# Optimization experiments

Measured on AMD Instinct MI355X. Metric: run time of the kernel, lower is better.

Reference implementation:

```python
import jax, jax.numpy as jnp
from jax import lax
import numpy as np

B, C_IN, H, W = 8, 1024, 64, 64
DI, C_OUT = 512, 1024
BN_EPS = 1e-5


def setup_inputs() -> dict:
    key = jax.random.key(0)
    ks = jax.random.split(key, 5)
    std = 0.01  # torch init.normal_(std=0.01)
    return {
        "x": jax.random.normal(ks[0], (B, C_IN, H, W), jnp.float32),
        "theta_w": jax.random.normal(ks[1], (DI, C_IN), jnp.float32) * std,
        "theta_b": jnp.zeros((DI,), jnp.float32),
        "phi_w": jax.random.normal(ks[2], (DI, C_IN), jnp.float32) * std,
        "phi_b": jnp.zeros((DI,), jnp.float32),
        "g_w": jax.random.normal(ks[3], (DI, C_IN), jnp.float32) * std,
        "g_b": jnp.zeros((DI,), jnp.float32),
        "out_w": jax.random.normal(ks[4], (C_OUT, DI), jnp.float32) * std,
        "out_b": jnp.zeros((C_OUT,), jnp.float32),
        "bn_w": jnp.ones((C_OUT,), jnp.float32),
        "bn_b": jnp.zeros((C_OUT,), jnp.float32),
    }


def _conv1x1(x, w, b):
    # x: [b,c,h,w], w: [o,c] -> [b,o,h,w]
    return jnp.einsum('bchw,oc->bohw', x, w) + b[None, :, None, None]


def reference(x, theta_w, theta_b, phi_w, phi_b, g_w, g_b, out_w, out_b, bn_w, bn_b):
    b, c, h, w = x.shape
    di = theta_w.shape[0]

    theta = _conv1x1(x, theta_w, theta_b).reshape(b, di, h * w)  # [b,di,N]

    # MaxPool2d(kernel=2, stride=2)
    pool = lax.reduce_window(x, -jnp.inf, lax.max,
                             (1, 1, 2, 2), (1, 1, 2, 2), 'VALID')
    phi = _conv1x1(pool, phi_w, phi_b).reshape(b, di, -1)   # [b,di,M]
    g = _conv1x1(pool, g_w, g_b).reshape(b, di, -1)          # [b,di,M]

    # scaled dot-product attention: scores [b,N,M]
    scores = jnp.einsum('bdn,bdm->bnm', theta, phi) * (di ** -0.5)
    p = jax.nn.softmax(scores, axis=-1)

    # t_x = g @ p^T  -> [b,di,N]
    t = jnp.einsum('bdm,bnm->bdn', g, p).reshape(b, di, h, w)

    y = _conv1x1(t, out_w, out_b)  # [b,C_out,h,w]

    # BatchNorm2d (training mode: batch statistics, biased variance)
    mean = jnp.mean(y, axis=(0, 2, 3), keepdims=True)
    var = jnp.var(y, axis=(0, 2, 3), keepdims=True)
    y = (y - mean) * lax.rsqrt(var + BN_EPS)
    y = y * bn_w[None, :, None, None] + bn_b[None, :, None, None]

    return y + x
```

## Files before the change

kernel.cpp:

```cpp
#include <hip/hip_runtime.h>
#include <cstdint>

typedef unsigned short u16;
typedef __attribute__((ext_vector_type(4))) unsigned short u16x4;
typedef __attribute__((ext_vector_type(8))) short short8;
typedef __attribute__((ext_vector_type(4))) float f32x4;

#define DI 512
#define CIN 1024
#define NPIX 4096
#define MPIX 1024

__device__ __forceinline__ float bf2f(u16 u) {
  union { unsigned int i; float f; } v; v.i = ((unsigned int)u) << 16; return v.f;
}
__device__ __forceinline__ u16 f2bf(float f) {
  union { float f; unsigned int i; } v; v.f = f;
  unsigned int r = v.i + 0x7fffu + ((v.i >> 16) & 1u);
  return (u16)(r >> 16);
}
__device__ __forceinline__ void unpack8(uint4 v, float* f) {
  union { unsigned int i; float f; } u;
  u.i = v.x << 16;          f[0] = u.f;
  u.i = v.x & 0xffff0000u;  f[1] = u.f;
  u.i = v.y << 16;          f[2] = u.f;
  u.i = v.y & 0xffff0000u;  f[3] = u.f;
  u.i = v.z << 16;          f[4] = u.f;
  u.i = v.z & 0xffff0000u;  f[5] = u.f;
  u.i = v.w << 16;          f[6] = u.f;
  u.i = v.w & 0xffff0000u;  f[7] = u.f;
}

__device__ __forceinline__ void gload16(const u16* g, u16* l) {
  __builtin_amdgcn_global_load_lds(
      (const __attribute__((address_space(1))) void*)g,
      (__attribute__((address_space(3))) void*)l, 16, 0, 0);
}

__global__ __launch_bounds__(256) void cvt4_kernel(
    const float* __restrict__ s0, const float* __restrict__ s1,
    const float* __restrict__ s2, const float* __restrict__ s3,
    u16* __restrict__ d0, u16* __restrict__ d1,
    u16* __restrict__ d2, u16* __restrict__ d3) {
  int i = blockIdx.x * 256 + threadIdx.x;
  int sel = i >> 17;
  int j = i & 131071;
  const float* src = sel == 0 ? s0 : sel == 1 ? s1 : sel == 2 ? s2 : s3;
  u16* dst = sel == 0 ? d0 : sel == 1 ? d1 : sel == 2 ? d2 : d3;
  float4 v = *(const float4*)(src + (long)j * 4);
  u16x4 w;
  w[0] = f2bf(v.x); w[1] = f2bf(v.y); w[2] = f2bf(v.z); w[3] = f2bf(v.w);
  *(u16x4*)(dst + (long)j * 4) = w;
}

__global__ __launch_bounds__(256) void transpose_kernel(const float* __restrict__ x,
                                                        u16* __restrict__ xT) {
  __shared__ u16 tile[64][72];
  const int b = blockIdx.z;
  const int n0 = blockIdx.x * 64, c0 = blockIdx.y * 64;
  const float* xb = x + (long)b * CIN * NPIX;
  u16* xTb = xT + (long)b * NPIX * CIN;
  const int t = threadIdx.x;
  const int tc = t >> 4, tn = (t & 15) * 4;
  #pragma unroll
  for (int i = 0; i < 4; i++) {
    int c = tc + i * 16;
    float4 v = *(const float4*)(xb + (long)(c0 + c) * NPIX + n0 + tn);
    tile[c][tn + 0] = f2bf(v.x);
    tile[c][tn + 1] = f2bf(v.y);
    tile[c][tn + 2] = f2bf(v.z);
    tile[c][tn + 3] = f2bf(v.w);
  }
  __syncthreads();
  const int tn2 = t >> 4, tc2 = (t & 15) * 4;
  #pragma unroll
  for (int i = 0; i < 4; i++) {
    int n = tn2 + i * 16;
    u16x4 w;
    w[0] = tile[tc2 + 0][n];
    w[1] = tile[tc2 + 1][n];
    w[2] = tile[tc2 + 2][n];
    w[3] = tile[tc2 + 3][n];
    *(u16x4*)(xTb + (long)(n0 + n) * CIN + c0 + tc2) = w;
  }
}

__global__ __launch_bounds__(256) void pool_kernel(const u16* __restrict__ xT,
                                                   u16* __restrict__ poolT) {
  const int idx = blockIdx.x * 256 + threadIdx.x;
  const int cc = (idx & 127) * 8;
  const int m = (idx >> 7) & 1023;
  const int b = idx >> 17;
  const int i = m >> 5, j = m & 31;
  const int n1 = (i * 2) * 64 + j * 2;
  const u16* base = xT + (long)b * NPIX * CIN + cc;
  uint4 v0 = *(const uint4*)(base + (long)(n1) * CIN);
  uint4 v1 = *(const uint4*)(base + (long)(n1 + 1) * CIN);
  uint4 v2 = *(const uint4*)(base + (long)(n1 + 64) * CIN);
  uint4 v3 = *(const uint4*)(base + (long)(n1 + 65) * CIN);
  float f0[8], f1[8], f2[8], f3[8];
  unpack8(v0, f0); unpack8(v1, f1); unpack8(v2, f2); unpack8(v3, f3);
  u16 r[8] __attribute__((aligned(16)));
  #pragma unroll
  for (int k = 0; k < 8; k++) {
    float mx = fmaxf(fmaxf(f0[k], f1[k]), fmaxf(f2[k], f3[k]));
    r[k] = f2bf(mx);
  }
  *(uint4*)(poolT + ((long)b * MPIX + m) * CIN + cc) = *(uint4*)r;
}

template<int OM, bool HAS_BIAS, bool HAS_CS, bool HAS_SHIFT, bool HAS_EXP>
__global__ __launch_bounds__(256)
void gemm_tn(const u16* __restrict__ A, const u16* __restrict__ B,
             void* __restrict__ Cv,
             const float* __restrict__ bias, long sBias,
             const float* __restrict__ cs, long sCS,
             const float* __restrict__ shift, long sShift,
             float* __restrict__ psum_out,
             float scale, int M, int N, int K, long sA, long sB, long sC)
{
  A += blockIdx.z * sA;
  B += blockIdx.z * sB;
  if (HAS_BIAS) bias += blockIdx.z * sBias;
  if (HAS_CS) cs += blockIdx.z * sCS;
  if (HAS_SHIFT) shift += blockIdx.z * sShift;
  const int bm = blockIdx.y * 128;
  const int bn = blockIdx.x * 128;
  __shared__ __align__(16) u16 As[128 * 64];
  __shared__ __align__(16) u16 Bs[128 * 64];
  __shared__ float psum[2][128];
  const int tid = threadIdx.x;
  const int lane = tid & 63;
  const int wave = tid >> 6;
  const int wm = (wave >> 1) * 64;
  const int wn = (wave & 1) * 64;
  const int lr = lane & 15;
  const int q  = lane >> 4;
  const int sxor = lane & 7;
  f32x4 acc[4][4] = {};

  const int swz = ((lane & 7) ^ (lane >> 3)) * 8;
  const long grow = 32 * wave + (lane >> 3);
  const u16* Ag = A + ((long)bm + grow) * K + swz;
  const u16* Bg = B + ((long)bn + grow) * K + swz;

  for (int kt = 0; kt < K; kt += 64) {
    __syncthreads();
    #pragma unroll
    for (int i = 0; i < 4; i++) {
      gload16(Ag + (long)(8 * i) * K + kt, &As[(wave * 4 + i) * 512]);
      gload16(Bg + (long)(8 * i) * K + kt, &Bs[(wave * 4 + i) * 512]);
    }
    __syncthreads();
    #pragma unroll
    for (int kk = 0; kk < 2; kk++) {
      short8 av[4], bv[4];
      #pragma unroll
      for (int mi = 0; mi < 4; mi++)
        av[mi] = *(const short8*)&As[(wm + mi * 16 + lr) * 64 +
                                     (((kk << 2) + q) ^ sxor) * 8];
      #pragma unroll
      for (int ni = 0; ni < 4; ni++)
        bv[ni] = *(const short8*)&Bs[(wn + ni * 16 + lr) * 64 +
                                     (((kk << 2) + q) ^ sxor) * 8];
      #pragma unroll
      for (int mi = 0; mi < 4; mi++) {
        #pragma unroll
        for (int ni = 0; ni < 4; ni++)
          acc[mi][ni] = __builtin_amdgcn_mfma_f32_16x16x32_bf16(
              av[mi], bv[ni], acc[mi][ni], 0, 0, 0);
      }
    }
  }

  const int dr = (lane >> 4) * 4;
  float rowsum[4][4];
  if (HAS_EXP) {
    #pragma unroll
    for (int mi = 0; mi < 4; mi++)
      #pragma unroll
      for (int r = 0; r < 4; r++) rowsum[mi][r] = 0.f;
  }
  #pragma unroll
  for (int mi = 0; mi < 4; mi++) {
    const int rowb = bm + wm + mi * 16 + dr;
    float bvs[4] = {0.f, 0.f, 0.f, 0.f};
    float shv[4] = {0.f, 0.f, 0.f, 0.f};
    if (HAS_BIAS) {
      #pragma unroll
      for (int r = 0; r < 4; r++) bvs[r] = bias[rowb + r];
    }
    if (HAS_SHIFT) {
      #pragma unroll
      for (int r = 0; r < 4; r++) shv[r] = shift[rowb + r];
    }
    #pragma unroll
    for (int ni = 0; ni < 4; ni++) {
      const int col = bn + wn + ni * 16 + lr;
      const float csv = HAS_CS ? cs[col] : 1.0f;
      float v[4];
      #pragma unroll
      for (int r = 0; r < 4; r++) {
        float t = acc[mi][ni][r] * scale;
        if (HAS_CS) t *= csv;
        if (HAS_SHIFT) t -= shv[r];
        if (HAS_BIAS) t += bvs[r];
        if (HAS_EXP) { t = expf(t); rowsum[mi][r] += t; }
        v[r] = t;
      }
      if (OM == 1) {
        u16* C = (u16*)Cv + blockIdx.z * sC;
        u16x4 w;
        #pragma unroll
        for (int r = 0; r < 4; r++) w[r] = f2bf(v[r]);
        *(u16x4*)(C + (long)col * M + rowb) = w;
      } else if (OM == 0) {
        u16* C = (u16*)Cv + blockIdx.z * sC;
        #pragma unroll
        for (int r = 0; r < 4; r++)
          C[(long)(rowb + r) * N + col] = f2bf(v[r]);
      } else {
        float* C = (float*)Cv + blockIdx.z * sC;
        #pragma unroll
        for (int r = 0; r < 4; r++)
          C[(long)(rowb + r) * N + col] = v[r];
      }
    }
  }
  if (HAS_EXP) {
    #pragma unroll
    for (int msk = 1; msk < 16; msk <<= 1)
      #pragma unroll
      for (int mi = 0; mi < 4; mi++)
        #pragma unroll
        for (int r = 0; r < 4; r++)
          rowsum[mi][r] += __shfl_xor(rowsum[mi][r], msk);
    if ((lane & 15) == 0) {
      #pragma unroll
      for (int mi = 0; mi < 4; mi++)
        #pragma unroll
        for (int r = 0; r < 4; r++)
          psum[wave & 1][wm + mi * 16 + dr + r] = rowsum[mi][r];
    }
    __syncthreads();
    if (tid < 128)
      psum_out[((long)blockIdx.z * gridDim.x + blockIdx.x) * 4096 + bm + tid] =
          psum[0][tid] + psum[1][tid];
  }
}

__global__ __launch_bounds__(256) void inv_kernel(const float* __restrict__ partial,
                                                  float* __restrict__ inv) {
  const int idx = blockIdx.x * 256 + threadIdx.x;
  const int b = idx >> 12, n = idx & 4095;
  const float* p = partial + (long)b * 32768 + n;
  float s = 0.f;
  #pragma unroll
  for (int x = 0; x < 8; x++) s += p[(long)x * 4096];
  inv[idx] = 1.0f / s;
}

__global__ __launch_bounds__(256) void gbar_kernel(const u16* __restrict__ g_n,
                                                   float* __restrict__ gbar) {
  const int row = blockIdx.x * 4 + (threadIdx.x >> 6);
  const int lane = threadIdx.x & 63;
  const long base = (long)row * MPIX + lane * 16;
  uint4 va = *(const uint4*)(g_n + base);
  uint4 vb = *(const uint4*)(g_n + base + 8);
  float f[16];
  unpack8(va, f); unpack8(vb, f + 8);
  float s = 0.f;
  #pragma unroll
  for (int j = 0; j < 16; j++) s += f[j];
  #pragma unroll
  for (int off = 32; off > 0; off >>= 1) s += __shfl_xor(s, off);
  if (lane == 0) gbar[row] = s * (1.0f / 1024.0f);
}

__global__ __launch_bounds__(256) void c0_kernel(const float* __restrict__ out_w,
                                                 const float* __restrict__ out_b,
                                                 const float* __restrict__ gbar,
                                                 float* __restrict__ c0) {
  const int idx = blockIdx.x * 4 + (threadIdx.x >> 6);
  const int lane = threadIdx.x & 63;
  const int b = idx >> 10, c = idx & 1023;
  const int d0 = lane * 8;
  float4 w0 = *(const float4*)(out_w + (long)c * DI + d0);
  float4 w1 = *(const float4*)(out_w + (long)c * DI + d0 + 4);
  float4 g0 = *(const float4*)(gbar + (long)b * DI + d0);
  float4 g1 = *(const float4*)(gbar + (long)b * DI + d0 + 4);
  float s = w0.x * g0.x + w0.y * g0.y + w0.z * g0.z + w0.w * g0.w
          + w1.x * g1.x + w1.y * g1.y + w1.z * g1.z + w1.w * g1.w;
  #pragma unroll
  for (int off = 32; off > 0; off >>= 1) s += __shfl_xor(s, off);
  if (lane == 0) c0[idx] = out_b[c] + s;
}

__global__ __launch_bounds__(256) void stats_kernel(const u16* __restrict__ dy,
                                                    const float* __restrict__ c0,
                                                    float* __restrict__ stats) {
  const int co = blockIdx.x;
  const int t = threadIdx.x;
  float sd = 0.f, sd2 = 0.f, sbc = 0.f;
  for (int b = 0; b < 8; b++) {
    const long base = ((long)b * 1024 + co) * 4096;
    float pb = 0.f, pb2 = 0.f;
    #pragma unroll
    for (int i = 0; i < 2; i++) {
      uint4 v = *(const uint4*)(dy + base + (long)(i * 256 + t) * 8);
      float f[8]; unpack8(v, f);
      #pragma unroll
      for (int k = 0; k < 8; k++) { pb += f[k]; pb2 += f[k] * f[k]; }
    }
    sd += pb; sd2 += pb2;
    sbc += c0[b * 1024 + co] * pb;
  }
  #pragma unroll
  for (int off = 32; off > 0; off >>= 1) {
    sd += __shfl_xor(sd, off);
    sd2 += __shfl_xor(sd2, off);
    sbc += __shfl_xor(sbc, off);
  }
  __shared__ float rs[4], rq[4], rb[4];
  if ((t & 63) == 0) { rs[t >> 6] = sd; rq[t >> 6] = sd2; rb[t >> 6] = sbc; }
  __syncthreads();
  if (t == 0) {
    float sdT = rs[0] + rs[1] + rs[2] + rs[3];
    float sd2T = rq[0] + rq[1] + rq[2] + rq[3];
    float sbcT = rb[0] + rb[1] + rb[2] + rb[3];
    float sc0 = 0.f, sc02 = 0.f;
    #pragma unroll
    for (int b = 0; b < 8; b++) {
      float c = c0[b * 1024 + co];
      sc0 += c; sc02 += c * c;
    }
    stats[co] = 4096.0f * sc0 + sdT;
    stats[1024 + co] = 4096.0f * sc02 + 2.0f * sbcT + sd2T;
  }
}

__global__ __launch_bounds__(256) void final_kernel(const u16* __restrict__ dy,
    const float* __restrict__ x, const float* __restrict__ stats,
    const float* __restrict__ c0,
    const float* __restrict__ bnw, const float* __restrict__ bnb,
    float* __restrict__ out) {
  const int bc = blockIdx.x;
  const int co = bc & 1023;
  const float mean = stats[co] * (1.0f / 32768.0f);
  const float var = stats[1024 + co] * (1.0f / 32768.0f) - mean * mean;
  const float inv = rsqrtf(var + 1e-5f) * bnw[co];
  const float addc = bnb[co] - mean * inv + c0[bc] * inv;
  const long base = (long)bc * 4096;
  const int t = threadIdx.x;
  #pragma unroll
  for (int i = 0; i < 2; i++) {
    const long off = base + (long)(i * 256 + t) * 8;
    uint4 v = *(const uint4*)(dy + off);
    float f[8]; unpack8(v, f);
    const float4 x0 = *(const float4*)(x + off);
    const float4 x1 = *(const float4*)(x + off + 4);
    float4 o0, o1;
    o0.x = f[0] * inv + addc + x0.x;
    o0.y = f[1] * inv + addc + x0.y;
    o0.z = f[2] * inv + addc + x0.z;
    o0.w = f[3] * inv + addc + x0.w;
    o1.x = f[4] * inv + addc + x1.x;
    o1.y = f[5] * inv + addc + x1.y;
    o1.z = f[6] * inv + addc + x1.z;
    o1.w = f[7] * inv + addc + x1.w;
    *(float4*)(out + off) = o0;
    *(float4*)(out + off + 4) = o1;
  }
}

extern "C" void kernel_launch(void* const* d_in, const int* in_sizes, int n_in,
                              void* d_out, int out_size, void* d_ws, size_t ws_size,
                              hipStream_t stream) {
  (void)in_sizes; (void)n_in; (void)out_size; (void)ws_size;
  const float* x       = (const float*)d_in[0];
  const float* theta_w = (const float*)d_in[1];
  const float* theta_b = (const float*)d_in[2];
  const float* phi_w   = (const float*)d_in[3];
  const float* phi_b   = (const float*)d_in[4];
  const float* g_w     = (const float*)d_in[5];
  const float* g_b     = (const float*)d_in[6];
  const float* out_w   = (const float*)d_in[7];
  const float* out_b   = (const float*)d_in[8];
  const float* bn_w    = (const float*)d_in[9];
  const float* bn_b    = (const float*)d_in[10];
  float* out = (float*)d_out;
  char* ws = (char*)d_ws;
  const size_t MB = 1024 * 1024;

  u16* xT     = (u16*)(ws + 0 * MB);
  u16* poolT  = (u16*)(ws + 64 * MB);
  u16* w_th   = (u16*)(ws + 80 * MB);
  u16* w_ph   = (u16*)(ws + 81 * MB);
  u16* w_g    = (u16*)(ws + 82 * MB);
  u16* thetaT = (u16*)(ws + 84 * MB);
  u16* phiT   = (u16*)(ws + 116 * MB);
  u16* g_n    = (u16*)(ws + 124 * MB);
  u16* e      = (u16*)(ws + 132 * MB);
  u16* tT     = (u16*)(ws + 196 * MB);
  u16* w_out  = (u16*)(ws + 228 * MB);
  float* inv_s = (float*)(ws + 229 * MB);
  float* gbar  = (float*)(ws + 229 * MB + 131072);
  float* c0b   = (float*)(ws + 229 * MB + 147456);
  float* stats = (float*)(ws + 229 * MB + 180224);
  float* partial = (float*)(ws + 230 * MB);
  u16* dy = xT;

  cvt4_kernel<<<2048, 256, 0, stream>>>(theta_w, phi_w, g_w, out_w,
                                        w_th, w_ph, w_g, w_out);
  transpose_kernel<<<dim3(64, 16, 8), 256, 0, stream>>>(x, xT);
  pool_kernel<<<4096, 256, 0, stream>>>(xT, poolT);
  gemm_tn<1, true, false, false, false><<<dim3(32, 4, 8), 256, 0, stream>>>(
      w_th, xT, thetaT, theta_b, 0L, nullptr, 0L, nullptr, 0L, nullptr,
      1.0f, 512, 4096, 1024, 0L, (long)NPIX * CIN, (long)NPIX * DI);
  gemm_tn<1, true, false, false, false><<<dim3(8, 4, 8), 256, 0, stream>>>(
      w_ph, poolT, phiT, phi_b, 0L, nullptr, 0L, nullptr, 0L, nullptr,
      1.0f, 512, 1024, 1024, 0L, (long)MPIX * CIN, (long)MPIX * DI);
  gemm_tn<0, true, false, false, false><<<dim3(8, 4, 8), 256, 0, stream>>>(
      w_g, poolT, g_n, g_b, 0L, nullptr, 0L, nullptr, 0L, nullptr,
      1.0f, 512, 1024, 1024, 0L, (long)MPIX * CIN, (long)DI * MPIX);
  gbar_kernel<<<1024, 256, 0, stream>>>(g_n, gbar);
  c0_kernel<<<2048, 256, 0, stream>>>(out_w, out_b, gbar, c0b);
  gemm_tn<0, false, false, false, true><<<dim3(8, 32, 8), 256, 0, stream>>>(
      thetaT, phiT, e, nullptr, 0L, nullptr, 0L, nullptr, 0L, partial,
      0.044194173824159216f, 4096, 1024, 512,
      (long)NPIX * DI, (long)MPIX * DI, (long)NPIX * MPIX);
  inv_kernel<<<128, 256, 0, stream>>>(partial, inv_s);
  gemm_tn<1, false, true, true, false><<<dim3(32, 4, 8), 256, 0, stream>>>(
      g_n, e, tT, nullptr, 0L, inv_s, 4096L, gbar, 512L, nullptr,
      1.0f, 512, 4096, 1024,
      (long)DI * MPIX, (long)NPIX * MPIX, (long)NPIX * DI);
  gemm_tn<0, false, false, false, false><<<dim3(32, 8, 8), 256, 0, stream>>>(
      w_out, tT, dy, nullptr, 0L, nullptr, 0L, nullptr, 0L, nullptr,
      1.0f, 1024, 4096, 512, 0L, (long)NPIX * DI, (long)1024 * NPIX);
  stats_kernel<<<1024, 256, 0, stream>>>(dy, c0b, stats);
  final_kernel<<<8192, 256, 0, stream>>>(dy, x, stats, c0b, bn_w, bn_b, out);
}
```

Before: 380.2 us.

## Fuse maxpool into transpose and BN statistics into output GEMM epilogue

The transpose kernel now handles 128-pixel tiles (two image rows) and computes the 2x2 max pool from the shared tile, removing the separate pool pass that re-read xT. The output projection GEMM accumulates per-row sums and sums of squares in its epilogue and writes per-block partials. A small stats kernel then reduces these partials instead of re-reading the full dy tensor. This removes two large memory passes, at the cost of a bigger shared tile, extra epilogue work and shuffles, and a tiny serial reduction kernel.

```diff
diff --git a/kernel.cpp b/kernel.cpp
--- a/kernel.cpp
+++ b/kernel.cpp
@@ -53,18 +53,18 @@
   *(u16x4*)(dst + (long)j * 4) = w;
 }
 
-__global__ __launch_bounds__(256) void transpose_kernel(const float* __restrict__ x,
-                                                        u16* __restrict__ xT) {
-  __shared__ u16 tile[64][72];
+__global__ __launch_bounds__(256) void transpose_pool_kernel(
+    const float* __restrict__ x, u16* __restrict__ xT, u16* __restrict__ poolT) {
+  __shared__ u16 tile[64][136];
   const int b = blockIdx.z;
-  const int n0 = blockIdx.x * 64, c0 = blockIdx.y * 64;
+  const int n0 = blockIdx.x * 128, c0 = blockIdx.y * 64;
   const float* xb = x + (long)b * CIN * NPIX;
   u16* xTb = xT + (long)b * NPIX * CIN;
   const int t = threadIdx.x;
-  const int tc = t >> 4, tn = (t & 15) * 4;
-  #pragma unroll
-  for (int i = 0; i < 4; i++) {
-    int c = tc + i * 16;
+  const int tc = t >> 5, tn = (t & 31) * 4;
+  #pragma unroll
+  for (int i = 0; i < 8; i++) {
+    int c = tc + i * 8;
     float4 v = *(const float4*)(xb + (long)(c0 + c) * NPIX + n0 + tn);
     tile[c][tn + 0] = f2bf(v.x);
     tile[c][tn + 1] = f2bf(v.y);
@@ -74,7 +74,7 @@
   __syncthreads();
   const int tn2 = t >> 4, tc2 = (t & 15) * 4;
   #pragma unroll
-  for (int i = 0; i < 4; i++) {
+  for (int i = 0; i < 8; i++) {
     int n = tn2 + i * 16;
     u16x4 w;
     w[0] = tile[tc2 + 0][n];
@@ -83,33 +83,20 @@
     w[3] = tile[tc2 + 3][n];
     *(u16x4*)(xTb + (long)(n0 + n) * CIN + c0 + tc2) = w;
   }
-}
-
-__global__ __launch_bounds__(256) void pool_kernel(const u16* __restrict__ xT,
-                                                   u16* __restrict__ poolT) {
-  const int idx = blockIdx.x * 256 + threadIdx.x;
-  const int cc = (idx & 127) * 8;
-  const int m = (idx >> 7) & 1023;
-  const int b = idx >> 17;
-  const int i = m >> 5, j = m & 31;
-  const int n1 = (i * 2) * 64 + j * 2;
-  const u16* base = xT + (long)b * NPIX * CIN + cc;
-  uint4 v0 = *(const uint4*)(base + (long)(n1) * CIN);
-  uint4 v1 = *(const uint4*)(base + (long)(n1 + 1) * CIN);
-  uint4 v2 = *(const uint4*)(base + (long)(n1 + 64) * CIN);
-  uint4 v3 = *(const uint4*)(base + (long)(n1 + 65) * CIN);
-  float f0[8], f1[8], f2[8], f3[8];
-  unpack8(v0, f0); unpack8(v1, f1); unpack8(v2, f2); unpack8(v3, f3);
+  const int j = t >> 3, c8 = (t & 7) * 8;
   u16 r[8] __attribute__((aligned(16)));
   #pragma unroll
   for (int k = 0; k < 8; k++) {
-    float mx = fmaxf(fmaxf(f0[k], f1[k]), fmaxf(f2[k], f3[k]));
-    r[k] = f2bf(mx);
-  }
-  *(uint4*)(poolT + ((long)b * MPIX + m) * CIN + cc) = *(uint4*)r;
-}
-
-template<int OM, bool HAS_BIAS, bool HAS_CS, bool HAS_SHIFT, bool HAS_EXP>
+    int c = c8 + k;
+    float m0 = fmaxf(bf2f(tile[c][2 * j]), bf2f(tile[c][2 * j + 1]));
+    float m1 = fmaxf(bf2f(tile[c][64 + 2 * j]), bf2f(tile[c][64 + 2 * j + 1]));
+    r[k] = f2bf(fmaxf(m0, m1));
+  }
+  *(uint4*)(poolT + ((long)b * MPIX + blockIdx.x * 32 + j) * CIN + c0 + c8) =
+      *(uint4*)r;
+}
+
+template<int OM, bool HAS_BIAS, bool HAS_CS, bool HAS_SHIFT, bool HAS_EXP, bool HAS_PSUM2>
 __global__ __launch_bounds__(256)
 void gemm_tn(const u16* __restrict__ A, const u16* __restrict__ B,
              void* __restrict__ Cv,
@@ -128,7 +115,7 @@
   const int bn = blockIdx.x * 128;
   __shared__ __align__(16) u16 As[128 * 64];
   __shared__ __align__(16) u16 Bs[128 * 64];
-  __shared__ float psum[2][128];
+  __shared__ float psum[4][128];
   const int tid = threadIdx.x;
   const int lane = tid & 63;
   const int wave = tid >> 6;
@@ -175,11 +162,12 @@
 
   const int dr = (lane >> 4) * 4;
   float rowsum[4][4];
-  if (HAS_EXP) {
+  float rowsq[4][4];
+  if (HAS_EXP || HAS_PSUM2) {
     #pragma unroll
     for (int mi = 0; mi < 4; mi++)
       #pragma unroll
-      for (int r = 0; r < 4; r++) rowsum[mi][r] = 0.f;
+      for (int r = 0; r < 4; r++) { rowsum[mi][r] = 0.f; rowsq[mi][r] = 0.f; }
   }
   #pragma unroll
   for (int mi = 0; mi < 4; mi++) {
@@ -205,7 +193,9 @@
         if (HAS_CS) t *= csv;
         if (HAS_SHIFT) t -= shv[r];
         if (HAS_BIAS) t += bvs[r];
-        if (HAS_EXP) { t = expf(t); rowsum[mi][r] += t; }
+        if (HAS_EXP) t = expf(t);
+        if (HAS_EXP || HAS_PSUM2) rowsum[mi][r] += t;
+        if (HAS_PSUM2) rowsq[mi][r] += t * t;
         v[r] = t;
       }
       if (OM == 1) {
@@ -227,25 +217,37 @@
       }
     }
   }
-  if (HAS_EXP) {
+  if (HAS_EXP || HAS_PSUM2) {
     #pragma unroll
     for (int msk = 1; msk < 16; msk <<= 1)
       #pragma unroll
       for (int mi = 0; mi < 4; mi++)
         #pragma unroll
-        for (int r = 0; r < 4; r++)
+        for (int r = 0; r < 4; r++) {
           rowsum[mi][r] += __shfl_xor(rowsum[mi][r], msk);
+          if (HAS_PSUM2) rowsq[mi][r] += __shfl_xor(rowsq[mi][r], msk);
+        }
     if ((lane & 15) == 0) {
       #pragma unroll
       for (int mi = 0; mi < 4; mi++)
         #pragma unroll
-        for (int r = 0; r < 4; r++)
+        for (int r = 0; r < 4; r++) {
           psum[wave & 1][wm + mi * 16 + dr + r] = rowsum[mi][r];
+          if (HAS_PSUM2) psum[2 + (wave & 1)][wm + mi * 16 + dr + r] = rowsq[mi][r];
+        }
     }
     __syncthreads();
-    if (tid < 128)
-      psum_out[((long)blockIdx.z * gridDim.x + blockIdx.x) * 4096 + bm + tid] =
-          psum[0][tid] + psum[1][tid];
+    if (tid < 128) {
+      if (HAS_EXP)
+        psum_out[((long)blockIdx.z * gridDim.x + blockIdx.x) * 4096 + bm + tid] =
+            psum[0][tid] + psum[1][tid];
+      if (HAS_PSUM2) {
+        const long blk = ((long)blockIdx.z * gridDim.y + blockIdx.y) * gridDim.x
+                         + blockIdx.x;
+        psum_out[blk * 256 + tid] = psum[0][tid] + psum[1][tid];
+        psum_out[blk * 256 + 128 + tid] = psum[2][tid] + psum[3][tid];
+      }
+    }
   }
 }
 
@@ -296,47 +298,31 @@
   if (lane == 0) c0[idx] = out_b[c] + s;
 }
 
-__global__ __launch_bounds__(256) void stats_kernel(const u16* __restrict__ dy,
-                                                    const float* __restrict__ c0,
-                                                    float* __restrict__ stats) {
-  const int co = blockIdx.x;
-  const int t = threadIdx.x;
+__global__ __launch_bounds__(256) void stats2_kernel(const float* __restrict__ partial,
+                                                     const float* __restrict__ c0,
+                                                     float* __restrict__ stats) {
+  const int co = blockIdx.x * 256 + threadIdx.x;
+  const int by = co >> 7, r = co & 127;
   float sd = 0.f, sd2 = 0.f, sbc = 0.f;
   for (int b = 0; b < 8; b++) {
-    const long base = ((long)b * 1024 + co) * 4096;
-    float pb = 0.f, pb2 = 0.f;
-    #pragma unroll
-    for (int i = 0; i < 2; i++) {
-      uint4 v = *(const uint4*)(dy + base + (long)(i * 256 + t) * 8);
-      float f[8]; unpack8(v, f);
-      #pragma unroll
-      for (int k = 0; k < 8; k++) { pb += f[k]; pb2 += f[k] * f[k]; }
-    }
-    sd += pb; sd2 += pb2;
-    sbc += c0[b * 1024 + co] * pb;
-  }
-  #pragma unroll
-  for (int off = 32; off > 0; off >>= 1) {
-    sd += __shfl_xor(sd, off);
-    sd2 += __shfl_xor(sd2, off);
-    sbc += __shfl_xor(sbc, off);
-  }
-  __shared__ float rs[4], rq[4], rb[4];
-  if ((t & 63) == 0) { rs[t >> 6] = sd; rq[t >> 6] = sd2; rb[t >> 6] = sbc; }
-  __syncthreads();
-  if (t == 0) {
-    float sdT = rs[0] + rs[1] + rs[2] + rs[3];
-    float sd2T = rq[0] + rq[1] + rq[2] + rq[3];
-    float sbcT = rb[0] + rb[1] + rb[2] + rb[3];
-    float sc0 = 0.f, sc02 = 0.f;
-    #pragma unroll
-    for (int b = 0; b < 8; b++) {
-      float c = c0[b * 1024 + co];
-      sc0 += c; sc02 += c * c;
-    }
-    stats[co] = 4096.0f * sc0 + sdT;
-    stats[1024 + co] = 4096.0f * sc02 + 2.0f * sbcT + sd2T;
-  }
+    float sb = 0.f, qb = 0.f;
+    #pragma unroll
+    for (int bx = 0; bx < 32; bx++) {
+      const long blk = (((long)b * 8 + by) * 32 + bx) * 256;
+      sb += partial[blk + r];
+      qb += partial[blk + 128 + r];
+    }
+    sd += sb; sd2 += qb;
+    sbc += c0[b * 1024 + co] * sb;
+  }
+  float sc0 = 0.f, sc02 = 0.f;
+  #pragma unroll
+  for (int b = 0; b < 8; b++) {
+    float c = c0[b * 1024 + co];
+    sc0 += c; sc02 += c * c;
+  }
+  stats[co] = 4096.0f * sc0 + sd;
+  stats[1024 + co] = 4096.0f * sc02 + 2.0f * sbc + sd2;
 }
 
 __global__ __launch_bounds__(256) void final_kernel(const u16* __restrict__ dy,
@@ -408,35 +394,35 @@
   float* c0b   = (float*)(ws + 229 * MB + 147456);
   float* stats = (float*)(ws + 229 * MB + 180224);
   float* partial = (float*)(ws + 230 * MB);
+  float* partial2 = (float*)(ws + 231 * MB);
   u16* dy = xT;
 
   cvt4_kernel<<<2048, 256, 0, stream>>>(theta_w, phi_w, g_w, out_w,
                                         w_th, w_ph, w_g, w_out);
-  transpose_kernel<<<dim3(64, 16, 8), 256, 0, stream>>>(x, xT);
-  pool_kernel<<<4096, 256, 0, stream>>>(xT, poolT);
-  gemm_tn<1, true, false, false, false><<<dim3(32, 4, 8), 256, 0, stream>>>(
+  transpose_pool_kernel<<<dim3(32, 16, 8), 256, 0, stream>>>(x, xT, poolT);
+  gemm_tn<1, true, false, false, false, false><<<dim3(32, 4, 8), 256, 0, stream>>>(
       w_th, xT, thetaT, theta_b, 0L, nullptr, 0L, nullptr, 0L, nullptr,
       1.0f, 512, 4096, 1024, 0L, (long)NPIX * CIN, (long)NPIX * DI);
-  gemm_tn<1, true, false, false, false><<<dim3(8, 4, 8), 256, 0, stream>>>(
+  gemm_tn<1, true, false, false, false, false><<<dim3(8, 4, 8), 256, 0, stream>>>(
       w_ph, poolT, phiT, phi_b, 0L, nullptr, 0L, nullptr, 0L, nullptr,
       1.0f, 512, 1024, 1024, 0L, (long)MPIX * CIN, (long)MPIX * DI);
-  gemm_tn<0, true, false, false, false><<<dim3(8, 4, 8), 256, 0, stream>>>(
+  gemm_tn<0, true, false, false, false, false><<<dim3(8, 4, 8), 256, 0, stream>>>(
       w_g, poolT, g_n, g_b, 0L, nullptr, 0L, nullptr, 0L, nullptr,
       1.0f, 512, 1024, 1024, 0L, (long)MPIX * CIN, (long)DI * MPIX);
   gbar_kernel<<<1024, 256, 0, stream>>>(g_n, gbar);
   c0_kernel<<<2048, 256, 0, stream>>>(out_w, out_b, gbar, c0b);
-  gemm_tn<0, false, false, false, true><<<dim3(8, 32, 8), 256, 0, stream>>>(
+  gemm_tn<0, false, false, false, true, false><<<dim3(8, 32, 8), 256, 0, stream>>>(
       thetaT, phiT, e, nullptr, 0L, nullptr, 0L, nullptr, 0L, partial,
       0.044194173824159216f, 4096, 1024, 512,
       (long)NPIX * DI, (long)MPIX * DI, (long)NPIX * MPIX);
   inv_kernel<<<128, 256, 0, stream>>>(partial, inv_s);
-  gemm_tn<1, false, true, true, false><<<dim3(32, 4, 8), 256, 0, stream>>>(
+  gemm_tn<1, false, true, true, false, false><<<dim3(32, 4, 8), 256, 0, stream>>>(
       g_n, e, tT, nullptr, 0L, inv_s, 4096L, gbar, 512L, nullptr,
       1.0f, 512, 4096, 1024,
       (long)DI * MPIX, (long)NPIX * MPIX, (long)NPIX * DI);
-  gemm_tn<0, false, false, false, false><<<dim3(32, 8, 8), 256, 0, stream>>>(
-      w_out, tT, dy, nullptr, 0L, nullptr, 0L, nullptr, 0L, nullptr,
+  gemm_tn<0, false, false, false, false, true><<<dim3(32, 8, 8), 256, 0, stream>>>(
+      w_out, tT, dy, nullptr, 0L, nullptr, 0L, nullptr, 0L, partial2,
       1.0f, 1024, 4096, 512, 0L, (long)NPIX * DI, (long)1024 * NPIX);
-  stats_kernel<<<1024, 256, 0, stream>>>(dy, c0b, stats);
+  stats2_kernel<<<4, 256, 0, stream>>>(partial2, c0b, stats);
   final_kernel<<<8192, 256, 0, stream>>>(dy, x, stats, c0b, bn_w, bn_b, out);
 }
```

Result: no change. 387.4 us (+1.9%).
